# Optimization experiments

Hardware: AMD Instinct MI355X
Metric: run time of the kernel (lower is better)

## Reference

```python
import jax, jax.numpy as jnp
import numpy as np

B, T, S, D, H, FF = 4, 1024, 1024, 1024, 16, 4096
DH = D // H
NEG = -1e9
EPS = 1e-5


def setup_inputs() -> dict:
    key = jax.random.key(0)
    ks = jax.random.split(key, 20)
    p = 0.02  # param init scale
    inp = {
        "x": jax.random.normal(ks[0], (B, T, D), jnp.float32),
        "encoder_output": jax.random.normal(ks[1], (B, S, D), jnp.float32),
        "src_mask": jnp.ones((B, 1, 1, S), jnp.bool_),
        "tgt_mask": jnp.tril(jnp.ones((1, 1, T, T), jnp.bool_)),  # causal
        # self-attention params
        "d_Wq": jax.random.normal(ks[2], (D, D)) * p, "d_bq": jnp.zeros((D,)),
        "d_Wk": jax.random.normal(ks[3], (D, D)) * p, "d_bk": jnp.zeros((D,)),
        "d_Wv": jax.random.normal(ks[4], (D, D)) * p, "d_bv": jnp.zeros((D,)),
        "d_Wo": jax.random.normal(ks[5], (D, D)) * p, "d_bo": jnp.zeros((D,)),
        # cross-attention params
        "e_Wq": jax.random.normal(ks[6], (D, D)) * p, "e_bq": jnp.zeros((D,)),
        "e_Wk": jax.random.normal(ks[7], (D, D)) * p, "e_bk": jnp.zeros((D,)),
        "e_Wv": jax.random.normal(ks[8], (D, D)) * p, "e_bv": jnp.zeros((D,)),
        "e_Wo": jax.random.normal(ks[9], (D, D)) * p, "e_bo": jnp.zeros((D,)),
        # FFN params
        "ff_W1": jax.random.normal(ks[10], (D, FF)) * p, "ff_b1": jnp.zeros((FF,)),
        "ff_W2": jax.random.normal(ks[11], (FF, D)) * p, "ff_b2": jnp.zeros((D,)),
        # layernorm params
        "ln1_g": jnp.ones((D,)), "ln1_b": jnp.zeros((D,)),
        "ln2_g": jnp.ones((D,)), "ln2_b": jnp.zeros((D,)),
        "ln3_g": jnp.ones((D,)), "ln3_b": jnp.zeros((D,)),
    }
    return inp


def _mha(xq, xkv, Wq, bq, Wk, bk, Wv, bv, Wo, bo, mask):
    b, tq = xq.shape[0], xq.shape[1]
    q = (xq @ Wq + bq).reshape(b, tq, H, DH).transpose(0, 2, 1, 3)
    k = (xkv @ Wk + bk).reshape(b, -1, H, DH).transpose(0, 2, 1, 3)
    v = (xkv @ Wv + bv).reshape(b, -1, H, DH).transpose(0, 2, 1, 3)
    scores = jnp.einsum("bhqd,bhkd->bhqk", q, k) / np.float32(np.sqrt(DH))
    scores = jnp.where(mask, scores, NEG)
    attn = jax.nn.softmax(scores, axis=-1)
    out = jnp.einsum("bhqk,bhkd->bhqd", attn, v)
    out = out.transpose(0, 2, 1, 3).reshape(b, tq, D)
    return out @ Wo + bo


def _ln(x, g, b):
    m = jnp.mean(x, axis=-1, keepdims=True)
    v = jnp.var(x, axis=-1, keepdims=True)
    return (x - m) / jnp.sqrt(v + EPS) * g + b


def reference(x, encoder_output, src_mask, tgt_mask,
              d_Wq, d_bq, d_Wk, d_bk, d_Wv, d_bv, d_Wo, d_bo,
              e_Wq, e_bq, e_Wk, e_bk, e_Wv, e_bv, e_Wo, e_bo,
              ff_W1, ff_b1, ff_W2, ff_b2,
              ln1_g, ln1_b, ln2_g, ln2_b, ln3_g, ln3_b):
    # masked self-attention + residual + LN (dropout is identity in eval)
    d = _mha(x, x, d_Wq, d_bq, d_Wk, d_bk, d_Wv, d_bv, d_Wo, d_bo, tgt_mask)
    d = _ln(d + x, ln1_g, ln1_b)
    # cross-attention over encoder output + residual + LN
    f = _mha(d, encoder_output, e_Wq, e_bq, e_Wk, e_bk, e_Wv, e_bv, e_Wo, e_bo, src_mask)
    f = _ln(f + d, ln2_g, ln2_b)
    # FFN + residual + LN
    g = jax.nn.relu(f @ ff_W1 + ff_b1) @ ff_W2 + ff_b2
    g = _ln(g + f, ln3_g, ln3_b)
    return g
```

## Files before the change

### kernel.cpp

```cpp
#include <hip/hip_runtime.h>

static constexpr int Bc = 4, Tc = 1024, Sc = 1024, Dc = 1024, Hc = 16, DHc = 64, FFc = 4096;

typedef __attribute__((ext_vector_type(8))) short short8;
typedef __attribute__((ext_vector_type(4))) short short4v;
typedef __attribute__((ext_vector_type(4))) float f32x4;

struct P8 { unsigned short* o[8]; };

__device__ __forceinline__ unsigned short f2bf(float f) {
    unsigned int u = __float_as_uint(f);
    unsigned int r = u + 0x7fffu + ((u >> 16) & 1u);
    return (unsigned short)(r >> 16);
}
__device__ __forceinline__ float bf2f(unsigned short u) {
    return __uint_as_float(((unsigned int)u) << 16);
}
__device__ __forceinline__ float fexp2(float x) {
    float r; asm("v_exp_f32 %0, %1" : "=v"(r) : "v"(x)); return r;
}
__device__ __forceinline__ unsigned int cvtpk(float a, float b) {
    unsigned int r;
    asm("v_cvt_pk_bf16_f32 %0, %1, %2" : "=v"(r) : "v"(a), "v"(b));
    return r;
}

__device__ __forceinline__ void gload_lds16(const void* g, void* l) {
    __builtin_amdgcn_global_load_lds((const __attribute__((address_space(1))) void*)g,
                                     (__attribute__((address_space(3))) void*)l, 16, 0, 0);
}

__global__ __launch_bounds__(256) void cast2_f32_bf16(const float* __restrict__ inA,
                                                      const float* __restrict__ inB,
                                                      unsigned short* __restrict__ outA,
                                                      unsigned short* __restrict__ outB, int n8) {
    int i = blockIdx.x * 256 + threadIdx.x;
    if (i >= n8) return;
    const float* in = blockIdx.y ? inB : inA;
    unsigned short* out = blockIdx.y ? outB : outA;
    const float4* p = (const float4*)in + (size_t)i * 2;
    float4 a = p[0], b = p[1];
    short8 o;
    o[0] = f2bf(a.x); o[1] = f2bf(a.y); o[2] = f2bf(a.z); o[3] = f2bf(a.w);
    o[4] = f2bf(b.x); o[5] = f2bf(b.y); o[6] = f2bf(b.z); o[7] = f2bf(b.w);
    *(short8*)(out + (size_t)i * 8) = o;
}

struct TJ { const float* s; unsigned short* d; int ss, ds; float scl; };
struct TJ16 { TJ j[16]; };
__global__ __launch_bounds__(256) void transpose_cast16(TJ16 p) {
    __shared__ float t[64][65];
    const TJ jb = p.j[blockIdx.z];
    const int c0 = blockIdx.x * 64, r0 = blockIdx.y * 64;
    const int tid = threadIdx.x;
    const int rr = tid >> 2, cc = (tid & 3) * 16;
    const float* src = jb.s + (size_t)(r0 + rr) * jb.ss + c0 + cc;
#pragma unroll
    for (int i = 0; i < 4; i++) {
        float4 v = *(const float4*)(src + i * 4);
        t[rr][cc + i * 4 + 0] = v.x;
        t[rr][cc + i * 4 + 1] = v.y;
        t[rr][cc + i * 4 + 2] = v.z;
        t[rr][cc + i * 4 + 3] = v.w;
    }
    __syncthreads();
#pragma unroll
    for (int half = 0; half < 2; half++) {
        const int id = half * 256 + tid;
        const int a = id >> 3, b0 = id & 7;
        short8 o;
#pragma unroll
        for (int e = 0; e < 8; e++) o[e] = f2bf(t[b0 * 8 + e][a] * jb.scl);
        *(short8*)(jb.d + (size_t)(c0 + a) * jb.ds + r0 + b0 * 8) = o;
    }
}

__global__ void prep_bias(const float* dbq, const float* dbk, const float* dbv,
                          const float* ebk, const float* ebv, const float* ebq,
                          float* __restrict__ bqkv, float* __restrict__ bekv,
                          float* __restrict__ ebq_s, float SC) {
    int i = blockIdx.x * 256 + threadIdx.x;
    int seg = i >> 10, j = i & 1023;
    switch (seg) {
        case 0: bqkv[j] = dbq[j] * SC; break;
        case 1: bqkv[1024 + j] = dbk[j]; break;
        case 2: bqkv[2048 + j] = dbv[j]; break;
        case 3: bekv[j] = ebk[j]; break;
        case 4: bekv[1024 + j] = ebv[j]; break;
        default: ebq_s[j] = ebq[j] * SC; break;
    }
}

__global__ __launch_bounds__(256) void combine2(unsigned short* __restrict__ dst,
                                                const unsigned short* __restrict__ p1, int n8) {
    int i = blockIdx.x * 256 + threadIdx.x;
    if (i >= n8) return;
    short8 a = *(short8*)(dst + (size_t)i * 8);
    short8 b = *(const short8*)(p1 + (size_t)i * 8);
    short8 o;
#pragma unroll
    for (int j = 0; j < 8; j++)
        o[j] = f2bf(bf2f((unsigned short)a[j]) + bf2f((unsigned short)b[j]));
    *(short8*)(dst + (size_t)i * 8) = o;
}

__global__ __launch_bounds__(256) void transpose_v(const unsigned short* __restrict__ V, int ldv,
                                                   unsigned short* __restrict__ Vt) {
    __shared__ unsigned short t[64 * 64];
    const int bh = blockIdx.y, b = bh >> 4, h = bh & 15;
    const int s0 = blockIdx.x * 64;
    const int tid = threadIdx.x;
    const int r = tid >> 2, ch = tid & 3;
    const unsigned short* src = V + (size_t)(b * 1024 + s0 + r) * ldv + h * 64 + ch * 16;
    short8 v0 = *(const short8*)src;
    short8 v1 = *(const short8*)(src + 8);
    int pw_ = (ch ^ r ^ (r >> 4)) & 3;
    *(short8*)(t + r * 64 + pw_ * 16) = v0;
    *(short8*)(t + r * 64 + pw_ * 16 + 8) = v1;
    __syncthreads();
    const int dh = tid >> 2, sc = (tid & 3) * 16;
    short8 o0, o1;
#pragma unroll
    for (int j = 0; j < 8; j++) {
        int c0 = sc + j, c1 = sc + 8 + j;
        o0[j] = t[c0 * 64 + (((dh >> 4) ^ c0 ^ (c0 >> 4)) & 3) * 16 + (dh & 15)];
        o1[j] = t[c1 * 64 + (((dh >> 4) ^ c1 ^ (c1 >> 4)) & 3) * 16 + (dh & 15)];
    }
    unsigned short* dst = Vt + ((size_t)bh * 64 + dh) * 1024 + s0 + sc;
    *(short8*)dst = o0;
    *(short8*)(dst + 8) = o1;
}

struct BlkMap { int m, n, z; };
__device__ __forceinline__ BlkMap remap_block() {
    const int gx = gridDim.x, gy = gridDim.y;
    const int nxy = gx * gy;
    const int nwg = nxy * gridDim.z;
    const int flat = (blockIdx.z * gy + blockIdx.y) * gx + blockIdx.x;
    const int id = (flat & 7) * (nwg >> 3) + (flat >> 3);
    const int pz = id / nxy;
    const int rz = id - pz * nxy;
    const int gwsh = (gx & 7) ? 2 : 3;
    const int gw = 1 << gwsh;
    const int gsz = gw * gy;
    const int grp = rz / gsz;
    const int rem = rz - grp * gsz;
    BlkMap r;
    r.m = rem >> gwsh;
    r.n = (grp << gwsh) + (rem & (gw - 1));
    r.z = pz;
    return r;
}

template <int EPI>
__global__ __launch_bounds__(512, 2) void gemm256(const unsigned short* __restrict__ A,
                                                  const unsigned short* __restrict__ Bt,
                                                  const float* __restrict__ bias,
                                                  unsigned short* __restrict__ outB,
                                                  int N, int lda, int ldb, int nk, P8 po) {
    __shared__ unsigned short SM[2][2][2][8192];
    const int tid = threadIdx.x;
    const int lane = tid & 63, wid = tid >> 6;
    const int l4 = lane & 15, g = lane >> 4;
    const int wr = wid >> 2, wc = wid & 3;
    BlkMap bm = remap_block();
    const int m0 = bm.m * 256, n0 = bm.n * 256, z = bm.z;
    A += (size_t)z * (nk * 64);
    Bt += (size_t)z * (nk * 64);
    const int sw = l4 & 7;

    const int fl0 = tid, fl1 = 512 + tid;
    const int lr0 = fl0 >> 3, ch0 = (fl0 & 7) ^ (lr0 & 7);
    const int lr1 = fl1 >> 3, ch1 = (fl1 & 7) ^ (lr1 & 7);
    const size_t A64 = (size_t)64 * lda;
    const unsigned short* pA0 = A + (size_t)(m0 + (lr0 >> 6) * 128 + (lr0 & 63)) * lda + ch0 * 8;
    const unsigned short* pA1 = A + (size_t)(m0 + (lr1 >> 6) * 128 + (lr1 & 63)) * lda + ch1 * 8;
    const unsigned short* pB0 = Bt + (size_t)(n0 + (ch0 >> 2) * 128 + lr0) * ldb + (ch0 & 3) * 8;
    const unsigned short* pB1 = Bt + (size_t)(n0 + (ch1 >> 2) * 128 + lr1) * ldb + (ch1 & 3) * 8;

    auto stA = [&](int d, int mh, int kofs) {
        char* base = (char*)&SM[0][d][mh][0];
        gload_lds16(pA0 + (size_t)mh * A64 + kofs, base + fl0 * 16);
        gload_lds16(pA1 + (size_t)mh * A64 + kofs, base + fl1 * 16);
    };
    auto stB = [&](int d, int ks, int kofs) {
        char* base = (char*)&SM[1][d][ks][0];
        gload_lds16(pB0 + ks * 32 + kofs, base + fl0 * 16);
        gload_lds16(pB1 + ks * 32 + kofs, base + fl1 * 16);
    };

    f32x4 acc[8][4] = {};
    short8 aF[4], aH[4], b0[4], b1[4];

    auto ldA = [&](int d, int mh, short8* d0, short8* d1) {
#pragma unroll
        for (int m = 0; m < 4; m++) {
            const char* rp = (const char*)&SM[0][d][mh][0] + (wr * 64 + m * 16 + l4) * 128;
            d0[m] = *(const short8*)(rp + ((g ^ sw) * 16));
            d1[m] = *(const short8*)(rp + (((4 + g) ^ sw) * 16));
        }
    };
    auto ldB = [&](int d, int ks, short8* dst) {
#pragma unroll
        for (int n = 0; n < 4; n++) {
            const char* rp = (const char*)&SM[1][d][ks][0] + ((wc & 1) * 64 + n * 16 + l4) * 128;
            dst[n] = *(const short8*)(rp + ((((wc >> 1) * 4 + g) ^ sw) * 16));
        }
    };

#define MFMA16(aa, bb, base)                                                                  \
    _Pragma("unroll") for (int m_ = 0; m_ < 4; m_++)                                          \
        _Pragma("unroll") for (int n_ = 0; n_ < 4; n_++)                                      \
            acc[(base) + m_][n_] = __builtin_amdgcn_mfma_f32_16x16x32_bf16(                   \
                (aa)[m_], (bb)[n_], acc[(base) + m_][n_], 0, 0, 0);

    stB(0, 0, 0); stA(0, 0, 0); stB(0, 1, 0); stA(0, 1, 0);
    stB(1, 0, 64); stA(1, 0, 64); stB(1, 1, 64);
    asm volatile("s_waitcnt vmcnt(6)" ::: "memory");
    __builtin_amdgcn_s_barrier();

    const int nIter = nk >> 1;
    for (int it = 0; it < nIter; ++it) {
        const int t = 2 * it, u = t + 1;
        const int ku = u * 64;
        const int kv = ((t + 2 < nk) ? t + 2 : t) * 64;
        const int kw = ((u + 2 < nk) ? u + 2 : u) * 64;
        ldB(0, 0, b0); ldA(0, 0, aF, aH);
        stA(1, 1, ku);
        asm volatile("s_waitcnt lgkmcnt(8)" ::: "memory");
        __builtin_amdgcn_s_barrier();
        asm volatile("s_waitcnt lgkmcnt(0)" ::: "memory");
        __builtin_amdgcn_s_setprio(1); MFMA16(aF, b0, 0); __builtin_amdgcn_s_setprio(0);
        __builtin_amdgcn_s_barrier();
        ldB(0, 1, b1);
        stB(0, 0, kv);
        __builtin_amdgcn_s_barrier();
        asm volatile("s_waitcnt lgkmcnt(0)" ::: "memory");
        __builtin_amdgcn_s_setprio(1); MFMA16(aH, b1, 0); __builtin_amdgcn_s_setprio(0);
        __builtin_amdgcn_s_barrier();
        ldA(0, 1, aF, aH);
        stA(0, 0, kv);
        __builtin_amdgcn_s_barrier();
        asm volatile("s_waitcnt lgkmcnt(0)" ::: "memory");
        __builtin_amdgcn_s_setprio(1); MFMA16(aH, b1, 4); __builtin_amdgcn_s_setprio(0);
        __builtin_amdgcn_s_barrier();
        stB(0, 1, kv);
        __builtin_amdgcn_s_barrier();
        __builtin_amdgcn_s_setprio(1); MFMA16(aF, b0, 4); __builtin_amdgcn_s_setprio(0);
        asm volatile("s_waitcnt vmcnt(6)" ::: "memory");
        __builtin_amdgcn_s_barrier();
        ldB(1, 0, b0); ldA(1, 0, aF, aH);
        stA(0, 1, kv);
        asm volatile("s_waitcnt lgkmcnt(8)" ::: "memory");
        __builtin_amdgcn_s_barrier();
        asm volatile("s_waitcnt lgkmcnt(0)" ::: "memory");
        __builtin_amdgcn_s_setprio(1); MFMA16(aF, b0, 0); __builtin_amdgcn_s_setprio(0);
        __builtin_amdgcn_s_barrier();
        ldB(1, 1, b1);
        stB(1, 0, kw);
        __builtin_amdgcn_s_barrier();
        asm volatile("s_waitcnt lgkmcnt(0)" ::: "memory");
        __builtin_amdgcn_s_setprio(1); MFMA16(aH, b1, 0); __builtin_amdgcn_s_setprio(0);
        __builtin_amdgcn_s_barrier();
        ldA(1, 1, aF, aH);
        stA(1, 0, kw);
        __builtin_amdgcn_s_barrier();
        asm volatile("s_waitcnt lgkmcnt(0)" ::: "memory");
        __builtin_amdgcn_s_setprio(1); MFMA16(aH, b1, 4); __builtin_amdgcn_s_setprio(0);
        __builtin_amdgcn_s_barrier();
        stB(1, 1, kw);
        __builtin_amdgcn_s_barrier();
        __builtin_amdgcn_s_setprio(1); MFMA16(aF, b0, 4); __builtin_amdgcn_s_setprio(0);
        asm volatile("s_waitcnt vmcnt(6)" ::: "memory");
        __builtin_amdgcn_s_barrier();
    }
    asm volatile("s_waitcnt vmcnt(0)" ::: "memory");
    __syncthreads();

    unsigned short* eb = (unsigned short*)SM;
    unsigned short* oB = (EPI == 3) ? po.o[z] : outB;
    const int colL = wc * 64 + l4;
#pragma unroll
    for (int h = 0; h < 2; ++h) {
        if (wr == h) {
#pragma unroll
            for (int mm = 0; mm < 8; mm++) {
                const int base_r = (mm < 4 ? mm * 16 : 64 + (mm - 4) * 16) + g * 4;
#pragma unroll
                for (int n = 0; n < 4; n++) {
                    float bv = (EPI == 3 && z != 0) ? 0.f : bias[n0 + colL + n * 16];
#pragma unroll
                    for (int r = 0; r < 4; r++) {
                        float v = acc[mm][n][r] + bv;
                        if (EPI == 2) v = fmaxf(v, 0.f);
                        eb[(base_r + r) * 260 + colL + n * 16] = f2bf(v);
                    }
                }
            }
        }
        __syncthreads();
        const int gr0 = m0 + h * 128;
#pragma unroll
        for (int j = 0; j < 8; j++) {
            const int f = j * 8192 + tid * 16;
            const int row = f >> 9;
            const int colb = f & 511;
            short8 v = *(const short8*)((const char*)eb + row * 520 + colb);
            *(short8*)(oB + (size_t)(gr0 + row) * N + n0 + (colb >> 1)) = v;
        }
        if (h == 0) __syncthreads();
    }
#undef MFMA16
}

template <int EPI>
__global__ __launch_bounds__(256) void gemm64_db(const unsigned short* __restrict__ A,
                                                 const unsigned short* __restrict__ Bt,
                                                 const float* __restrict__ bias,
                                                 float* __restrict__ outF,
                                                 unsigned short* __restrict__ outB,
                                                 int M, int N, int Kloop, int lda, int ldb) {
    __shared__ unsigned short As[3][64 * 32];
    __shared__ unsigned short Bs[3][128 * 32];
    const int tid = threadIdx.x;
    const int w = tid >> 6, lane = tid & 63, l4 = lane & 15, g = lane >> 4;
    BlkMap bm = remap_block();
    const int m0 = bm.m * 64, n0 = bm.n * 128;
    f32x4 acc[4][2] = {};
    const int r0 = tid >> 2;
    const int kk = ((tid & 3) ^ ((tid >> 3) & 3)) * 8;
    const int sk = (l4 >> 1) & 3;
    const unsigned short* Ar0 = A + (size_t)(m0 + r0) * lda + kk;
    const unsigned short* Br0 = Bt + (size_t)(n0 + r0) * ldb + kk;
    const unsigned short* Br1 = Bt + (size_t)(n0 + 64 + r0) * ldb + kk;
    auto stage = [&](int sb, int k0) {
        gload_lds16(Ar0 + k0, (char*)As[sb] + tid * 16);
        gload_lds16(Br0 + k0, (char*)Bs[sb] + tid * 16);
        gload_lds16(Br1 + k0, (char*)Bs[sb] + 4096 + tid * 16);
    };
    const int nk = Kloop >> 5;
    stage(0, 0);
    stage(1, 32);
    asm volatile("s_waitcnt vmcnt(3)" ::: "memory");
    __builtin_amdgcn_s_barrier();
    asm volatile("" ::: "memory");
    int buf = 0;
    for (int t = 0; t < nk; ++t) {
        if (t + 2 < nk) {
            int b2 = buf + 2; if (b2 >= 3) b2 -= 3;
            stage(b2, (t + 2) * 32);
        }
        short8 a[4], b[2];
#pragma unroll
        for (int m = 0; m < 4; m++)
            a[m] = *(const short8*)(As[buf] + (m * 16 + l4) * 32 + (g ^ sk) * 8);
#pragma unroll
        for (int n = 0; n < 2; n++)
            b[n] = *(const short8*)(Bs[buf] + (w * 32 + n * 16 + l4) * 32 + (g ^ sk) * 8);
#pragma unroll
        for (int m = 0; m < 4; m++)
#pragma unroll
            for (int n = 0; n < 2; n++)
                acc[m][n] = __builtin_amdgcn_mfma_f32_16x16x32_bf16(a[m], b[n], acc[m][n], 0, 0, 0);
        if (t + 1 < nk) {
            if (t + 2 < nk) asm volatile("s_waitcnt vmcnt(3)" ::: "memory");
            else            asm volatile("s_waitcnt vmcnt(0)" ::: "memory");
            __builtin_amdgcn_s_barrier();
            asm volatile("" ::: "memory");
        }
        buf = (buf + 1 == 3) ? 0 : buf + 1;
    }
    const int rowB = m0 + g * 4;
    const int colB = n0 + w * 32 + l4;
#pragma unroll
    for (int n = 0; n < 2; n++) {
        float bv = bias[colB + n * 16];
#pragma unroll
        for (int m = 0; m < 4; m++) {
#pragma unroll
            for (int r = 0; r < 4; r++) {
                float v = acc[m][n][r] + bv;
                if (EPI == 2) v = fmaxf(v, 0.f);
                size_t idx = (size_t)(rowB + m * 16 + r) * N + colB + n * 16;
                if (EPI == 1) outF[idx] = v;
                else outB[idx] = f2bf(v);
            }
        }
    }
}

template <int CAUSAL>
__global__ __launch_bounds__(512) void attn6_kernel(const unsigned short* __restrict__ Q, int ldq,
                                                    const unsigned short* __restrict__ Kg, int ldk,
                                                    const unsigned short* __restrict__ Vt,
                                                    unsigned short* __restrict__ O) {
    __shared__ unsigned short Kl[2 * 64 * 64];
    __shared__ unsigned short Vl[2 * 64 * 64];
    __shared__ unsigned short Pl[8][16 * 72];
    const int bh = blockIdx.x;
    const int qb = CAUSAL ? (gridDim.y - 1 - blockIdx.y) : blockIdx.y;
    const int b = bh >> 4, h = bh & 15;
    const int tid = threadIdx.x, w = tid >> 6, lane = tid & 63;
    const int l4 = lane & 15, g = lane >> 4;
    const int q0 = qb * 128 + w * 16;
    const unsigned short* Qp = Q + (size_t)(b * Tc + q0 + l4) * ldq + h * DHc + g * 8;
    short8 qf0 = *(const short8*)Qp;
    short8 qf1 = *(const short8*)(Qp + 32);
    const unsigned short* Kbase = Kg + (size_t)(b * 1024) * ldk + h * DHc;
    const unsigned short* Vbase = Vt + (size_t)bh * DHc * 1024;
    f32x4 o[4] = {};
    float mrun = -1e30f, lrun = 0.f;
    const int nT = CAUSAL ? 2 * qb + 2 : 16;
    unsigned short* pw = &Pl[w][l4 * 72];
    const int qi = q0 + l4;

    short8 ones;
#pragma unroll
    for (int j = 0; j < 8; j++) ones[j] = (short)0x3F80;

    const int sr = tid >> 3;
    const int sc_ = (tid & 7) ^ (sr & 7);

    auto stage = [&](int s0, int buf) {
        char* kd = (char*)Kl + buf * 8192;
        char* vd = (char*)Vl + buf * 8192;
        gload_lds16(Kbase + (size_t)(s0 + sr) * ldk + sc_ * 8, kd + tid * 16);
        gload_lds16(Vbase + (size_t)sr * 1024 + s0 + sc_ * 8, vd + tid * 16);
    };

    stage(0, 0);
    __syncthreads();
    int buf = 0;
    const int sw = l4 & 7;

    for (int t = 0; t < nT; ++t) {
        const int s0 = t * 64;
        if (t + 1 < nT) stage(s0 + 64, buf ^ 1);
        if (!CAUSAL || s0 <= q0 + 15) {
            const unsigned short* Kb_ = Kl + buf * 4096;
            const unsigned short* Vb_ = Vl + buf * 4096;
            f32x4 st[4];
            f32x4 z = {0.f, 0.f, 0.f, 0.f};
            __builtin_amdgcn_s_setprio(1);
#pragma unroll
            for (int c = 0; c < 4; c++) {
                const unsigned short* kr = Kb_ + (c * 16 + l4) * 64;
                short8 ka0 = *(const short8*)(kr + ((g ^ sw) * 8));
                short8 ka1 = *(const short8*)(kr + (((g + 4) ^ sw) * 8));
                st[c] = __builtin_amdgcn_mfma_f32_16x16x32_bf16(ka0, qf0, z, 0, 0, 0);
                st[c] = __builtin_amdgcn_mfma_f32_16x16x32_bf16(ka1, qf1, st[c], 0, 0, 0);
            }
            __builtin_amdgcn_s_setprio(0);
            float p[16];
            const bool domask = CAUSAL && (s0 + 63 > q0);
#pragma unroll
            for (int c = 0; c < 4; c++)
#pragma unroll
                for (int r = 0; r < 4; r++) {
                    float v = st[c][r];
                    if (domask && (s0 + c * 16 + g * 4 + r) > qi) v = -1e9f;
                    p[c * 4 + r] = v;
                }
            float m1 = fmaxf(fmaxf(p[0], p[1]), p[2]);
            float m2 = fmaxf(fmaxf(p[3], p[4]), p[5]);
            float m3 = fmaxf(fmaxf(p[6], p[7]), p[8]);
            float m4 = fmaxf(fmaxf(p[9], p[10]), p[11]);
            float m5 = fmaxf(fmaxf(p[12], p[13]), p[14]);
            float tmax = fmaxf(fmaxf(fmaxf(m1, m2), fmaxf(m3, m4)), fmaxf(m5, p[15]));
            tmax = fmaxf(tmax, __shfl_xor(tmax, 16));
            tmax = fmaxf(tmax, __shfl_xor(tmax, 32));
            if (!__all(tmax <= mrun + 11.5f)) {
                float mnew = fmaxf(mrun, tmax);
                float al = fexp2(mrun - mnew);
                lrun *= al;
#pragma unroll
                for (int d = 0; d < 4; d++) o[d] *= al;
                mrun = mnew;
            }
#pragma unroll
            for (int i = 0; i < 16; i++) p[i] = fexp2(p[i] - mrun);
#pragma unroll
            for (int c = 0; c < 4; c++) {
                uint2 u;
                u.x = cvtpk(p[c * 4 + 0], p[c * 4 + 1]);
                u.y = cvtpk(p[c * 4 + 2], p[c * 4 + 3]);
                *(uint2*)(pw + c * 16 + g * 4) = u;
            }
            short8 pb_lo = *(const short8*)(pw + g * 8);
            short8 pb_hi = *(const short8*)(pw + 32 + g * 8);
            __builtin_amdgcn_s_setprio(1);
            f32x4 s4 = __builtin_amdgcn_mfma_f32_16x16x32_bf16(ones, pb_lo, z, 0, 0, 0);
            s4 = __builtin_amdgcn_mfma_f32_16x16x32_bf16(ones, pb_hi, s4, 0, 0, 0);
#pragma unroll
            for (int d = 0; d < 4; d++) {
                const unsigned short* vr = Vb_ + (d * 16 + l4) * 64;
                short8 va0 = *(const short8*)(vr + ((g ^ sw) * 8));
                short8 va1 = *(const short8*)(vr + (((g + 4) ^ sw) * 8));
                o[d] = __builtin_amdgcn_mfma_f32_16x16x32_bf16(va0, pb_lo, o[d], 0, 0, 0);
                o[d] = __builtin_amdgcn_mfma_f32_16x16x32_bf16(va1, pb_hi, o[d], 0, 0, 0);
            }
            __builtin_amdgcn_s_setprio(0);
            lrun += s4[0];
        }
        __syncthreads();
        buf ^= 1;
    }
    float inv = 1.f / lrun;
    unsigned short* Ob = O + (size_t)(b * Tc + q0 + l4) * Dc + h * DHc;
#pragma unroll
    for (int d = 0; d < 4; d++) {
#pragma unroll
        for (int r = 0; r < 4; r++) Ob[d * 16 + g * 4 + r] = f2bf(o[d][r] * inv);
    }
}

__global__ __launch_bounds__(256) void ln_bf(const unsigned short* __restrict__ a,
                                             const unsigned short* __restrict__ res,
                                             const float* __restrict__ gam,
                                             const float* __restrict__ bet,
                                             unsigned short* __restrict__ outB,
                                             float* __restrict__ outF) {
    int row = blockIdx.x, t = threadIdx.x;
    size_t base = (size_t)row * Dc + t * 4;
    short4v av = *(const short4v*)(a + base);
    short4v rv = *(const short4v*)(res + base);
    float x0 = bf2f((unsigned short)av[0]) + bf2f((unsigned short)rv[0]);
    float x1 = bf2f((unsigned short)av[1]) + bf2f((unsigned short)rv[1]);
    float x2 = bf2f((unsigned short)av[2]) + bf2f((unsigned short)rv[2]);
    float x3 = bf2f((unsigned short)av[3]) + bf2f((unsigned short)rv[3]);
    float s = x0 + x1 + x2 + x3;
    float ss = x0 * x0 + x1 * x1 + x2 * x2 + x3 * x3;
    for (int o = 1; o < 64; o <<= 1) { s += __shfl_xor(s, o); ss += __shfl_xor(ss, o); }
    __shared__ float S1[4], S2[4];
    int w = t >> 6;
    if ((t & 63) == 0) { S1[w] = s; S2[w] = ss; }
    __syncthreads();
    s = S1[0] + S1[1] + S1[2] + S1[3];
    ss = S2[0] + S2[1] + S2[2] + S2[3];
    float mean = s * (1.f / Dc);
    float var = ss * (1.f / Dc) - mean * mean;
    float rstd = rsqrtf(var + 1e-5f);
    int c = t * 4;
    float4 g4 = *(const float4*)(gam + c);
    float4 b4 = *(const float4*)(bet + c);
    float y0 = (x0 - mean) * rstd * g4.x + b4.x;
    float y1 = (x1 - mean) * rstd * g4.y + b4.y;
    float y2 = (x2 - mean) * rstd * g4.z + b4.z;
    float y3 = (x3 - mean) * rstd * g4.w + b4.w;
    if (outB) {
        short4v ob;
        ob[0] = f2bf(y0); ob[1] = f2bf(y1); ob[2] = f2bf(y2); ob[3] = f2bf(y3);
        *(short4v*)(outB + base) = ob;
    }
    if (outF) { float4 ov = {y0, y1, y2, y3}; *(float4*)(outF + base) = ov; }
}

__global__ __launch_bounds__(256) void ln_4b(const unsigned short* __restrict__ p,
                                             const unsigned short* __restrict__ res,
                                             const float* __restrict__ gam,
                                             const float* __restrict__ bet,
                                             float* __restrict__ outF) {
    const size_t PS = (size_t)4096 * 1024;
    int row = blockIdx.x, t = threadIdx.x;
    size_t base = (size_t)row * Dc + t * 4;
    float x0, x1, x2, x3;
    {
        short4v rv = *(const short4v*)(res + base);
        x0 = bf2f((unsigned short)rv[0]); x1 = bf2f((unsigned short)rv[1]);
        x2 = bf2f((unsigned short)rv[2]); x3 = bf2f((unsigned short)rv[3]);
    }
#pragma unroll
    for (int j = 0; j < 4; j++) {
        short4v v = *(const short4v*)(p + j * PS + base);
        x0 += bf2f((unsigned short)v[0]); x1 += bf2f((unsigned short)v[1]);
        x2 += bf2f((unsigned short)v[2]); x3 += bf2f((unsigned short)v[3]);
    }
    float s = x0 + x1 + x2 + x3;
    float ss = x0 * x0 + x1 * x1 + x2 * x2 + x3 * x3;
    for (int o = 1; o < 64; o <<= 1) { s += __shfl_xor(s, o); ss += __shfl_xor(ss, o); }
    __shared__ float S1[4], S2[4];
    int w = t >> 6;
    if ((t & 63) == 0) { S1[w] = s; S2[w] = ss; }
    __syncthreads();
    s = S1[0] + S1[1] + S1[2] + S1[3];
    ss = S2[0] + S2[1] + S2[2] + S2[3];
    float mean = s * (1.f / Dc);
    float var = ss * (1.f / Dc) - mean * mean;
    float rstd = rsqrtf(var + 1e-5f);
    int c = t * 4;
    float4 g4 = *(const float4*)(gam + c);
    float4 b4 = *(const float4*)(bet + c);
    float4 ov;
    ov.x = (x0 - mean) * rstd * g4.x + b4.x;
    ov.y = (x1 - mean) * rstd * g4.y + b4.y;
    ov.z = (x2 - mean) * rstd * g4.z + b4.z;
    ov.w = (x3 - mean) * rstd * g4.w + b4.w;
    *(float4*)(outF + base) = ov;
}

extern "C" void kernel_launch(void* const* d_in, const int* in_sizes, int n_in,
                              void* d_out, int out_size, void* d_ws, size_t ws_size,
                              hipStream_t stream) {
    const float* x   = (const float*)d_in[0];
    const float* enc = (const float*)d_in[1];
    const float* dWq = (const float*)d_in[4];  const float* dbq = (const float*)d_in[5];
    const float* dWk = (const float*)d_in[6];  const float* dbk = (const float*)d_in[7];
    const float* dWv = (const float*)d_in[8];  const float* dbv = (const float*)d_in[9];
    const float* dWo = (const float*)d_in[10]; const float* dbo = (const float*)d_in[11];
    const float* eWq = (const float*)d_in[12]; const float* ebq = (const float*)d_in[13];
    const float* eWk = (const float*)d_in[14]; const float* ebk = (const float*)d_in[15];
    const float* eWv = (const float*)d_in[16]; const float* ebv = (const float*)d_in[17];
    const float* eWo = (const float*)d_in[18]; const float* ebo = (const float*)d_in[19];
    const float* fW1 = (const float*)d_in[20]; const float* fb1 = (const float*)d_in[21];
    const float* fW2 = (const float*)d_in[22]; const float* fb2 = (const float*)d_in[23];
    const float* g1 = (const float*)d_in[24];  const float* be1 = (const float*)d_in[25];
    const float* g2 = (const float*)d_in[26];  const float* be2 = (const float*)d_in[27];
    const float* g3 = (const float*)d_in[28];  const float* be3 = (const float*)d_in[29];

    const float SC = 0.125f * 1.44269504f;

    char* ws = (char*)d_ws;
    size_t off = 0;
    auto alloc = [&](size_t bytes) -> void* {
        void* p = ws + off;
        off += (bytes + 255) & ~(size_t)255;
        return p;
    };
    const size_t A = (size_t)4096 * 1024;
    const size_t MB1 = (size_t)1024 * 1024;
    char* R1 = (char*)alloc(32 * 1024 * 1024);
    unsigned short* qkv = (unsigned short*)R1;
    unsigned short* kvx = (unsigned short*)R1;
    unsigned short* qx  = (unsigned short*)(R1 + 16 * 1024 * 1024);
    unsigned short* h1  = (unsigned short*)R1;
    unsigned short* xb   = (unsigned short*)alloc(A * 2);
    unsigned short* encb = (unsigned short*)alloc(A * 2);
    unsigned short* wqkv = (unsigned short*)alloc(3 * MB1 * 2);
    unsigned short* wekv = (unsigned short*)alloc(2 * MB1 * 2);
    unsigned short* weq  = (unsigned short*)alloc(MB1 * 2);
    unsigned short* wdo  = (unsigned short*)alloc(MB1 * 2);
    unsigned short* weo  = (unsigned short*)alloc(MB1 * 2);
    unsigned short* wf1  = (unsigned short*)alloc(4 * MB1 * 2);
    unsigned short* wf2  = (unsigned short*)alloc(4 * MB1 * 2);
    float* bqkv = (float*)alloc(3072 * 4);
    float* bekv = (float*)alloc(2048 * 4);
    float* ebq_s = (float*)alloc(1024 * 4);
    unsigned short* VtB = (unsigned short*)alloc(A * 2);
    unsigned short* ab  = (unsigned short*)alloc(A * 2);
    unsigned short* tmpB = (unsigned short*)alloc(A * 2);
    unsigned short* dB = (unsigned short*)alloc(A * 2);
    unsigned short* fB = (unsigned short*)alloc(A * 2);
    unsigned short* pfb = VtB;
    (void)ws_size; (void)in_sizes; (void)n_in; (void)out_size;

    cast2_f32_bf16<<<dim3(2048, 2), 256, 0, stream>>>(x, enc, xb, encb, (int)(A / 8));

    TJ16 tj;
    tj.j[0] = {dWq, wqkv,           1024, 1024, SC};
    tj.j[1] = {dWk, wqkv + MB1,     1024, 1024, 1.f};
    tj.j[2] = {dWv, wqkv + 2 * MB1, 1024, 1024, 1.f};
    tj.j[3] = {eWk, wekv,           1024, 1024, 1.f};
    tj.j[4] = {eWv, wekv + MB1,     1024, 1024, 1.f};
    tj.j[5] = {eWq, weq,            1024, 1024, SC};
    tj.j[6] = {dWo, wdo,            1024, 1024, 1.f};
    tj.j[7] = {eWo, weo,            1024, 1024, 1.f};
    for (int jj = 0; jj < 4; jj++) {
        tj.j[8 + jj]  = {fW1 + 1024 * jj, wf1 + (size_t)1024 * jj * 1024, 4096, 1024, 1.f};
        tj.j[12 + jj] = {fW2 + (size_t)1024 * jj * 1024, wf2 + 1024 * jj, 1024, 4096, 1.f};
    }
    transpose_cast16<<<dim3(16, 16, 16), 256, 0, stream>>>(tj);
    prep_bias<<<24, 256, 0, stream>>>(dbq, dbk, dbv, ebk, ebv, ebq, bqkv, bekv, ebq_s, SC);

    P8 z8{};

    gemm256<0><<<dim3(12, 16), 512, 0, stream>>>(xb, wqkv, bqkv, qkv, 3072, 1024, 1024, 16, z8);
    transpose_v<<<dim3(16, 64), 256, 0, stream>>>(qkv + 2048, 3072, VtB);
    attn6_kernel<1><<<dim3(64, 8), 512, 0, stream>>>(qkv, 3072, qkv + 1024, 3072, VtB, ab);
    gemm64_db<0><<<dim3(8, 64), 256, 0, stream>>>(ab, wdo, dbo, nullptr, tmpB, 4096, 1024, 1024, 1024, 1024);
    ln_bf<<<4096, 256, 0, stream>>>(tmpB, xb, g1, be1, dB, nullptr);

    {
        P8 pe{};
        pe.o[0] = kvx;
        pe.o[1] = VtB;
        gemm256<3><<<dim3(8, 16, 2), 512, 0, stream>>>(encb, wekv, bekv, nullptr, 2048, 1024, 1024, 8, pe);
        combine2<<<4096, 256, 0, stream>>>(kvx, VtB, (int)((size_t)4096 * 2048 / 8));
    }
    gemm64_db<0><<<dim3(8, 64), 256, 0, stream>>>(dB, weq, ebq_s, nullptr, qx, 4096, 1024, 1024, 1024, 1024);
    transpose_v<<<dim3(16, 64), 256, 0, stream>>>(kvx + 1024, 2048, VtB);
    attn6_kernel<0><<<dim3(64, 8), 512, 0, stream>>>(qx, 1024, kvx, 2048, VtB, ab);
    gemm64_db<0><<<dim3(8, 64), 256, 0, stream>>>(ab, weo, ebo, nullptr, tmpB, 4096, 1024, 1024, 1024, 1024);
    ln_bf<<<4096, 256, 0, stream>>>(tmpB, dB, g2, be2, fB, nullptr);

    gemm256<2><<<dim3(16, 16), 512, 0, stream>>>(fB, wf1, fb1, h1, 4096, 1024, 1024, 16, z8);
    {
        P8 pf{};
        pf.o[0] = pfb;
        pf.o[1] = pfb + A;
        pf.o[2] = pfb + 2 * A;
        pf.o[3] = pfb + 3 * A;
        gemm256<3><<<dim3(4, 16, 4), 512, 0, stream>>>(h1, wf2, fb2, nullptr, 1024, 4096, 4096, 16, pf);
    }
    ln_4b<<<4096, 256, 0, stream>>>(pfb, fB, g3, be3, (float*)d_out);
}
```

Before: 321.3 us.

## Fuse V transpose into QKV GEMM epilogue and into split-K KV combine

The self-attention QKV GEMM gets a new epilogue variant that writes the V columns directly in transposed per-head layout, so the separate transpose_v launch is no longer needed. For cross-attention, the split-K combine kernel and the V transpose are merged into one kernel: it sums the K half in place and writes the summed V straight into a transposed buffer (tmpB). This removes two launches and one round trip of V through global memory. The cost is strided, column-gathered stores from LDS in the GEMM epilogue, and tmpB is reused as the Vt buffer before the Wo GEMM overwrites it.

After: 320.1 us. About the same (-0.4%).

```diff
diff --git a/kernel.cpp b/kernel.cpp
--- a/kernel.cpp
+++ b/kernel.cpp
@@ -91,29 +91,40 @@
     }
 }
 
-__global__ __launch_bounds__(256) void combine2(unsigned short* __restrict__ dst,
-                                                const unsigned short* __restrict__ p1, int n8) {
-    int i = blockIdx.x * 256 + threadIdx.x;
-    if (i >= n8) return;
-    short8 a = *(short8*)(dst + (size_t)i * 8);
-    short8 b = *(const short8*)(p1 + (size_t)i * 8);
-    short8 o;
-#pragma unroll
-    for (int j = 0; j < 8; j++)
-        o[j] = f2bf(bf2f((unsigned short)a[j]) + bf2f((unsigned short)b[j]));
-    *(short8*)(dst + (size_t)i * 8) = o;
-}
-
-__global__ __launch_bounds__(256) void transpose_v(const unsigned short* __restrict__ V, int ldv,
-                                                   unsigned short* __restrict__ Vt) {
+__global__ __launch_bounds__(256) void combineKV(unsigned short* __restrict__ kv,
+                                                 const unsigned short* __restrict__ p1,
+                                                 unsigned short* __restrict__ Vt) {
     __shared__ unsigned short t[64 * 64];
-    const int bh = blockIdx.y, b = bh >> 4, h = bh & 15;
-    const int s0 = blockIdx.x * 64;
+    const int bx = blockIdx.x;
     const int tid = threadIdx.x;
+    if (bx < 2048) {
+        const int cid = bx * 256 + tid;
+        const int row = cid >> 7, col8 = (cid & 127) * 8;
+        const size_t a = (size_t)row * 2048 + col8;
+        short8 x = *(short8*)(kv + a);
+        short8 y = *(const short8*)(p1 + a);
+        short8 o;
+#pragma unroll
+        for (int j = 0; j < 8; j++)
+            o[j] = f2bf(bf2f((unsigned short)x[j]) + bf2f((unsigned short)y[j]));
+        *(short8*)(kv + a) = o;
+        return;
+    }
+    const int vb = bx - 2048;
+    const int bh = vb & 63, b = bh >> 4, h = bh & 15;
+    const int s0 = (vb >> 6) * 64;
     const int r = tid >> 2, ch = tid & 3;
-    const unsigned short* src = V + (size_t)(b * 1024 + s0 + r) * ldv + h * 64 + ch * 16;
-    short8 v0 = *(const short8*)src;
-    short8 v1 = *(const short8*)(src + 8);
+    const size_t off = (size_t)(b * 1024 + s0 + r) * 2048 + 1024 + h * 64 + ch * 16;
+    short8 x0 = *(const short8*)(kv + off);
+    short8 x1 = *(const short8*)(kv + off + 8);
+    short8 y0 = *(const short8*)(p1 + off);
+    short8 y1 = *(const short8*)(p1 + off + 8);
+    short8 v0, v1;
+#pragma unroll
+    for (int j = 0; j < 8; j++) {
+        v0[j] = f2bf(bf2f((unsigned short)x0[j]) + bf2f((unsigned short)y0[j]));
+        v1[j] = f2bf(bf2f((unsigned short)x1[j]) + bf2f((unsigned short)y1[j]));
+    }
     int pw_ = (ch ^ r ^ (r >> 4)) & 3;
     *(short8*)(t + r * 64 + pw_ * 16) = v0;
     *(short8*)(t + r * 64 + pw_ * 16 + 8) = v1;
@@ -300,13 +311,34 @@
         }
         __syncthreads();
         const int gr0 = m0 + h * 128;
-#pragma unroll
-        for (int j = 0; j < 8; j++) {
-            const int f = j * 8192 + tid * 16;
-            const int row = f >> 9;
-            const int colb = f & 511;
-            short8 v = *(const short8*)((const char*)eb + row * 520 + colb);
-            *(short8*)(oB + (size_t)(gr0 + row) * N + n0 + (colb >> 1)) = v;
+        if (EPI == 4 && n0 >= 2048) {
+            const int b_ = gr0 >> 10, sb = gr0 & 1023;
+#pragma unroll
+            for (int j = 0; j < 4; j++) {
+                const int id = j * 512 + tid;
+                const int col = id & 255, rseg = id >> 8;
+                const int rel = n0 - 2048 + col;
+                const int hh = rel >> 6, dh = rel & 63;
+                short8 v0, v1;
+#pragma unroll
+                for (int e = 0; e < 8; e++) {
+                    v0[e] = eb[(rseg * 16 + e) * 260 + col];
+                    v1[e] = eb[(rseg * 16 + 8 + e) * 260 + col];
+                }
+                unsigned short* dp = po.o[0] +
+                    ((size_t)(b_ * 16 + hh) * 64 + dh) * 1024 + sb + rseg * 16;
+                *(short8*)dp = v0;
+                *(short8*)(dp + 8) = v1;
+            }
+        } else {
+#pragma unroll
+            for (int j = 0; j < 8; j++) {
+                const int f = j * 8192 + tid * 16;
+                const int row = f >> 9;
+                const int colb = f & 511;
+                short8 v = *(const short8*)((const char*)eb + row * 520 + colb);
+                *(short8*)(oB + (size_t)(gr0 + row) * N + n0 + (colb >> 1)) = v;
+            }
         }
         if (h == 0) __syncthreads();
     }
@@ -673,8 +705,11 @@
 
     P8 z8{};
 
-    gemm256<0><<<dim3(12, 16), 512, 0, stream>>>(xb, wqkv, bqkv, qkv, 3072, 1024, 1024, 16, z8);
-    transpose_v<<<dim3(16, 64), 256, 0, stream>>>(qkv + 2048, 3072, VtB);
+    {
+        P8 pq{};
+        pq.o[0] = VtB;
+        gemm256<4><<<dim3(12, 16), 512, 0, stream>>>(xb, wqkv, bqkv, qkv, 3072, 1024, 1024, 16, pq);
+    }
     attn6_kernel<1><<<dim3(64, 8), 512, 0, stream>>>(qkv, 3072, qkv + 1024, 3072, VtB, ab);
     gemm64_db<0><<<dim3(8, 64), 256, 0, stream>>>(ab, wdo, dbo, nullptr, tmpB, 4096, 1024, 1024, 1024, 1024);
     ln_bf<<<4096, 256, 0, stream>>>(tmpB, xb, g1, be1, dB, nullptr);
@@ -684,11 +719,10 @@
         pe.o[0] = kvx;
         pe.o[1] = VtB;
         gemm256<3><<<dim3(8, 16, 2), 512, 0, stream>>>(encb, wekv, bekv, nullptr, 2048, 1024, 1024, 8, pe);
-        combine2<<<4096, 256, 0, stream>>>(kvx, VtB, (int)((size_t)4096 * 2048 / 8));
+        combineKV<<<3072, 256, 0, stream>>>(kvx, VtB, tmpB);
     }
     gemm64_db<0><<<dim3(8, 64), 256, 0, stream>>>(dB, weq, ebq_s, nullptr, qx, 4096, 1024, 1024, 1024, 1024);
-    transpose_v<<<dim3(16, 64), 256, 0, stream>>>(kvx + 1024, 2048, VtB);
-    attn6_kernel<0><<<dim3(64, 8), 512, 0, stream>>>(qx, 1024, kvx, 2048, VtB, ab);
+    attn6_kernel<0><<<dim3(64, 8), 512, 0, stream>>>(qx, 1024, kvx, 2048, tmpB, ab);
     gemm64_db<0><<<dim3(8, 64), 256, 0, stream>>>(ab, weo, ebo, nullptr, tmpB, 4096, 1024, 1024, 1024, 1024);
     ln_bf<<<4096, 256, 0, stream>>>(tmpB, dB, g2, be2, fB, nullptr);
 
```
